# Kernel tuning notes

Hardware: AMD Instinct MI355X
Metric: run time of the kernel (lower is better)

Reference implementation:

```python
import jax, jax.numpy as jnp
import numpy as np

B, T, D_IN, H, BR, D_OUT = 256, 500, 700, 200, 2, 35
V_TH = 1.0


def setup_inputs() -> dict:
    key = jax.random.key(0)
    ks = jax.random.split(key, 7)
    x = jax.random.normal(ks[0], (B, T, D_IN), dtype=jnp.float32)
    W_in = jax.random.normal(ks[1], (H * BR, D_IN), dtype=jnp.float32) * (1.0 / np.sqrt(D_IN))
    b_in = jax.random.normal(ks[2], (H * BR,), dtype=jnp.float32) * 0.01
    # tau_n ~ U(0, 4) per branch per neuron (as in SimpleDH_LIF init)
    tau_n = jax.random.uniform(ks[3], (H, BR), dtype=jnp.float32, minval=0.0, maxval=4.0)
    tau_m = jnp.full((H,), 2.0, dtype=jnp.float32)  # torch init: tensor(2.0) per neuron
    W_out = jax.random.normal(ks[5], (D_OUT, H), dtype=jnp.float32) * (1.0 / np.sqrt(H))
    b_out = jax.random.normal(ks[6], (D_OUT,), dtype=jnp.float32) * 0.01
    return {"x": x, "W_in": W_in, "b_in": b_in, "tau_n": tau_n,
            "tau_m": tau_m, "W_out": W_out, "b_out": b_out}


def reference(x, W_in, b_in, tau_n, tau_m, W_out, b_out):
    b, t, _ = x.shape
    # Batched input projection for all timesteps at once: (B,T,H*BR) -> (T,B,H,BR)
    branch_in = jnp.einsum('bti,oi->bto', x, W_in) + b_in
    branch_in = branch_in.reshape(b, t, H, BR).transpose(1, 0, 2, 3)

    beta = jax.nn.sigmoid(tau_n)          # (H, BR) dendritic branch decay
    alpha = jax.nn.sigmoid(tau_m)         # (H,)   soma membrane decay

    def step(carry, inp_t):
        v, i_d, counts = carry            # v:(B,H) i_d:(B,H,BR) counts:(B,H)
        i_d = beta * i_d + (1.0 - beta) * inp_t
        i_total = i_d.sum(axis=-1)        # (B,H)
        v = alpha * v + (1.0 - alpha) * i_total
        spike = (v >= V_TH).astype(v.dtype)
        v = v - spike * V_TH
        return (v, i_d, counts + spike), None

    v0 = jnp.zeros((b, H), dtype=x.dtype)
    i0 = jnp.zeros((b, H, BR), dtype=x.dtype)
    c0 = jnp.zeros((b, H), dtype=x.dtype)
    (v, i_d, spike_counts), _ = jax.lax.scan(step, (v0, i0, c0), branch_in)

    return spike_counts @ W_out.T + b_out  # (B, D_OUT)
```

## Files before the change

kernel.cpp:

```cpp
#include <hip/hip_runtime.h>

#define B_   256
#define T_   500
#define DIN  700
#define H_   200
#define NO   400
#define DOUT 35
#define NKC  22

typedef _Float16 half_t;
typedef __attribute__((ext_vector_type(8))) _Float16 half8;
typedef __attribute__((ext_vector_type(4))) float floatx4;

#define SX 16.0f
#define SW 4096.0f
#define INV_S (1.0f / 65536.0f)

__device__ __forceinline__ float sigmoidf_(float x) {
    return 1.0f / (1.0f + expf(-x));
}

__global__ __launch_bounds__(256) void cvt_wfrag(
    const float* __restrict__ W, half_t* __restrict__ Whf, half_t* __restrict__ Wlf)
{
    int t = blockIdx.x * 256 + threadIdx.x;
    if (t >= NKC * 25 * 64) return;
    int lane = t & 63;
    int rest = t >> 6;
    int nfg  = rest % 25;
    int kc   = rest / 25;
    int la = lane & 15, lb = lane >> 4;
    int row = nfg * 16 + la;
    int col = kc * 32 + lb * 8;
    half8 hh, ll;
    #pragma unroll
    for (int j = 0; j < 8; ++j) {
        float v = (col + j < DIN) ? W[(size_t)row * DIN + col + j] : 0.0f;
        float s = v * SW;
        half_t h = (half_t)s;
        hh[j] = h;
        ll[j] = (half_t)(s - (float)h);
    }
    *reinterpret_cast<half8*>(&Whf[(size_t)t * 8]) = hh;
    *reinterpret_cast<half8*>(&Wlf[(size_t)t * 8]) = ll;
}

__global__ __launch_bounds__(256, 1) void dh_gemm_ovl(
    const float* __restrict__ x,
    const half_t* __restrict__ Whf, const half_t* __restrict__ Wlf,
    const float* __restrict__ bin, float* __restrict__ Y)
{
    int p = blockIdx.x;
    int xcd = p & 7, slot = p >> 3;
    int L = (xcd < 4 ? xcd * 313 : 4 * 313 + (xcd - 4) * 312) + slot;

    const int w    = threadIdx.x >> 6;
    const int lane = threadIdx.x & 63;
    const int la   = lane & 15;
    const int lb   = lane >> 4;

    const int wave = L * 4 + w;
    const int mt = wave / 5, nt = wave - mt * 5;
    const int m0 = mt * 64;
    const int o0 = nt * 80;

    floatx4 acc[4][5];
    #pragma unroll
    for (int mf = 0; mf < 4; ++mf)
        #pragma unroll
        for (int nf = 0; nf < 5; ++nf) {
            floatx4 z = {0.f, 0.f, 0.f, 0.f};
            acc[mf][nf] = z;
        }

    size_t arow[4];
    #pragma unroll
    for (int mf = 0; mf < 4; ++mf)
        arow[mf] = (size_t)(m0 + mf * 16 + la) * DIN;
    const size_t bbase = ((size_t)(nt * 5) * 64 + lane) * 8;

    float4 aE[4][2], aO[4][2];
    half8 bEh[5], bEl[5], bOh[5], bOl[5];
    half8 fEh[4], fEl[4], fOh[4], fOl[4];

    auto LOADA = [&](float4 (&ra)[4][2], int kc) {
        if (kc > NKC - 1) kc = NKC - 1;
        const int col = kc * 32 + lb * 8;
        const int c2ofs = (col + 8 <= DIN) ? 4 : (692 - col);
        #pragma unroll
        for (int mf = 0; mf < 4; ++mf) {
            const float* ptr = &x[arow[mf] + col];
            ra[mf][0] = *reinterpret_cast<const float4*>(ptr);
            ra[mf][1] = *reinterpret_cast<const float4*>(ptr + c2ofs);
        }
    };
    auto LOADB = [&](half8 (&bh)[5], half8 (&bl)[5], int kc) {
        if (kc > NKC - 1) kc = NKC - 1;
        const size_t kofs = (size_t)kc * 25 * 64 * 8;
        #pragma unroll
        for (int nf = 0; nf < 5; ++nf) {
            size_t idx = bbase + kofs + (size_t)nf * 64 * 8;
            bh[nf] = *reinterpret_cast<const half8*>(&Whf[idx]);
            bl[nf] = *reinterpret_cast<const half8*>(&Wlf[idx]);
        }
    };
    auto CONV = [&](half8 (&fh)[4], half8 (&fl)[4], const float4 (&ra)[4][2]) {
        #pragma unroll
        for (int mf = 0; mf < 4; ++mf) {
            float vv[8];
            *reinterpret_cast<float4*>(&vv[0]) = ra[mf][0];
            *reinterpret_cast<float4*>(&vv[4]) = ra[mf][1];
            half8 hh, ll;
            #pragma unroll
            for (int j = 0; j < 8; ++j) {
                float s = vv[j] * SX;
                half_t h = (half_t)s;
                hh[j] = h;
                ll[j] = (half_t)(s - (float)h);
            }
            fh[mf] = hh;
            fl[mf] = ll;
        }
    };
    auto MFMAS = [&](const half8 (&fh)[4], const half8 (&fl)[4],
                     const half8 (&bh)[5], const half8 (&bl)[5]) {
        #pragma unroll
        for (int mf = 0; mf < 4; ++mf)
            #pragma unroll
            for (int nf = 0; nf < 5; ++nf)
                acc[mf][nf] = __builtin_amdgcn_mfma_f32_16x16x32_f16(fh[mf], bh[nf], acc[mf][nf], 0, 0, 0);
        #pragma unroll
        for (int mf = 0; mf < 4; ++mf)
            #pragma unroll
            for (int nf = 0; nf < 5; ++nf)
                acc[mf][nf] = __builtin_amdgcn_mfma_f32_16x16x32_f16(fh[mf], bl[nf], acc[mf][nf], 0, 0, 0);
        #pragma unroll
        for (int mf = 0; mf < 4; ++mf)
            #pragma unroll
            for (int nf = 0; nf < 5; ++nf)
                acc[mf][nf] = __builtin_amdgcn_mfma_f32_16x16x32_f16(fl[mf], bh[nf], acc[mf][nf], 0, 0, 0);
    };

#define SBAR() __builtin_amdgcn_sched_barrier(0)

    LOADA(aE, 0); SBAR();
    LOADB(bEh, bEl, 0); SBAR();
    LOADA(aO, 1); SBAR();
    LOADB(bOh, bOl, 1); SBAR();
    CONV(fEh, fEl, aE);
    SBAR();
    LOADA(aE, 2);
    SBAR();

    #pragma unroll 1
    for (int I = 0; I < 10; ++I) {
        const int kc = 2 * I;
        MFMAS(fEh, fEl, bEh, bEl);
        CONV(fOh, fOl, aO);
        SBAR();
        LOADB(bEh, bEl, kc + 2); SBAR();
        LOADA(aO, kc + 3); SBAR();
        MFMAS(fOh, fOl, bOh, bOl);
        CONV(fEh, fEl, aE);
        SBAR();
        LOADB(bOh, bOl, kc + 3); SBAR();
        LOADA(aE, kc + 4); SBAR();
    }
    MFMAS(fEh, fEl, bEh, bEl);
    CONV(fOh, fOl, aO);
    SBAR();
    MFMAS(fOh, fOl, bOh, bOl);

    float bo[5];
    #pragma unroll
    for (int nf = 0; nf < 5; ++nf) bo[nf] = bin[o0 + nf * 16 + la];

    #pragma unroll
    for (int mf = 0; mf < 4; ++mf) {
        int mbase = m0 + mf * 16 + lb * 4;
        #pragma unroll
        for (int rg = 0; rg < 4; ++rg) {
            int mm = mbase + rg;
            int bb = mm / T_;
            int tt = mm - bb * T_;
            float* yrow = &Y[((size_t)tt * B_ + bb) * NO + o0 + la];
            #pragma unroll
            for (int nf = 0; nf < 5; ++nf)
                yrow[nf * 16] = acc[mf][nf][rg] * INV_S + bo[nf];
        }
    }
#undef SBAR
}

#define BM 256
#define BN 64
#define BK 16
__global__ __launch_bounds__(256) void dh_gemm_in(
    const float* __restrict__ x, const float* __restrict__ Wt,
    const float* __restrict__ bin, float* __restrict__ Y)
{
    __shared__ float As[BK][BM + 4];
    __shared__ float Bs[BK][BN + 4];
    const int tid = threadIdx.x;
    const int tx = tid & 7;
    const int ty = tid >> 3;
    const int m0 = blockIdx.y * BM;
    const int o0 = blockIdx.x * BN;

    float acc[8][8];
    #pragma unroll
    for (int r = 0; r < 8; ++r)
        #pragma unroll
        for (int c = 0; c < 8; ++c) acc[r][c] = 0.0f;

    const int srow = tid >> 2;
    const int skq  = (tid & 3) << 2;

    for (int k0 = 0; k0 < DIN; k0 += BK) {
        float4 areg[4];
        #pragma unroll
        for (int i = 0; i < 4; ++i) {
            int idx = tid + i * 256;
            int row = idx >> 2;
            int kq  = (idx & 3) << 2;
            int kg  = k0 + kq;
            if (kg < DIN)
                areg[i] = *reinterpret_cast<const float4*>(&x[(size_t)(m0 + row) * DIN + kg]);
            else
                areg[i] = make_float4(0.f, 0.f, 0.f, 0.f);
        }
        float4 breg;
        {
            int kg = k0 + skq;
            int o  = o0 + srow;
            if (kg < DIN && o < NO)
                breg = *reinterpret_cast<const float4*>(&Wt[(size_t)o * DIN + kg]);
            else
                breg = make_float4(0.f, 0.f, 0.f, 0.f);
        }
        __syncthreads();
        #pragma unroll
        for (int i = 0; i < 4; ++i) {
            int idx = tid + i * 256;
            int row = idx >> 2;
            int kq  = (idx & 3) << 2;
            As[kq + 0][row] = areg[i].x;
            As[kq + 1][row] = areg[i].y;
            As[kq + 2][row] = areg[i].z;
            As[kq + 3][row] = areg[i].w;
        }
        Bs[skq + 0][srow] = breg.x;
        Bs[skq + 1][srow] = breg.y;
        Bs[skq + 2][srow] = breg.z;
        Bs[skq + 3][srow] = breg.w;
        __syncthreads();

        #pragma unroll
        for (int k = 0; k < BK; ++k) {
            float a[8], bb[8];
            *reinterpret_cast<float4*>(&a[0])  = *reinterpret_cast<const float4*>(&As[k][ty * 8]);
            *reinterpret_cast<float4*>(&a[4])  = *reinterpret_cast<const float4*>(&As[k][ty * 8 + 4]);
            *reinterpret_cast<float4*>(&bb[0]) = *reinterpret_cast<const float4*>(&Bs[k][tx * 8]);
            *reinterpret_cast<float4*>(&bb[4]) = *reinterpret_cast<const float4*>(&Bs[k][tx * 8 + 4]);
            #pragma unroll
            for (int r = 0; r < 8; ++r)
                #pragma unroll
                for (int c = 0; c < 8; ++c)
                    acc[r][c] = fmaf(a[r], bb[c], acc[r][c]);
        }
    }

    float bo[8];
    #pragma unroll
    for (int c = 0; c < 8; ++c) {
        int o = o0 + tx * 8 + c;
        bo[c] = (o < NO) ? bin[o] : 0.0f;
    }
    const int ob = o0 + tx * 8;
    if (ob < NO) {
        #pragma unroll
        for (int r = 0; r < 8; ++r) {
            int m = m0 + ty * 8 + r;
            int b = m / T_;
            int t = m - b * T_;
            float* yrow = &Y[((size_t)t * B_ + b) * NO];
            float4 v0 = make_float4(acc[r][0] + bo[0], acc[r][1] + bo[1],
                                    acc[r][2] + bo[2], acc[r][3] + bo[3]);
            float4 v1 = make_float4(acc[r][4] + bo[4], acc[r][5] + bo[5],
                                    acc[r][6] + bo[6], acc[r][7] + bo[7]);
            *reinterpret_cast<float4*>(&yrow[ob])     = v0;
            *reinterpret_cast<float4*>(&yrow[ob + 4]) = v1;
        }
    }
}

__global__ __launch_bounds__(64) void dh_scan(
    const float* __restrict__ Y, const float* __restrict__ tau_n,
    const float* __restrict__ tau_m, float* __restrict__ counts)
{
    int g = blockIdx.x * 64 + threadIdx.x;
    int b = g / H_;
    int h = g - b * H_;
    (void)b;
    float beta0 = sigmoidf_(tau_n[h * 2 + 0]);
    float beta1 = sigmoidf_(tau_n[h * 2 + 1]);
    float alpha = sigmoidf_(tau_m[h]);
    float omb0 = 1.0f - beta0, omb1 = 1.0f - beta1, oma = 1.0f - alpha;
    const float2* Yp = reinterpret_cast<const float2*>(Y);

    float v = 0.f, i0 = 0.f, i1 = 0.f, cnt = 0.f;
    #pragma unroll 1
    for (int t0 = 0; t0 < T_; t0 += 10) {
        float2 yb[10];
        #pragma unroll
        for (int j = 0; j < 10; ++j)
            yb[j] = Yp[(size_t)(t0 + j) * (B_ * H_) + g];
        #pragma unroll
        for (int j = 0; j < 10; ++j) {
            i0 = beta0 * i0 + omb0 * yb[j].x;
            i1 = beta1 * i1 + omb1 * yb[j].y;
            float it = i0 + i1;
            v = alpha * v + oma * it;
            if (v >= 1.0f) { v -= 1.0f; cnt += 1.0f; }
        }
    }
    counts[g] = cnt;
}

__global__ __launch_bounds__(64) void dh_out(
    const float* __restrict__ counts, const float* __restrict__ W_out,
    const float* __restrict__ b_out, float* __restrict__ out)
{
    int b = blockIdx.x;
    int o = threadIdx.x;
    if (o >= DOUT) return;
    float acc = b_out[o];
    const float* c = &counts[(size_t)b * H_];
    const float* w = &W_out[(size_t)o * H_];
    #pragma unroll 4
    for (int h = 0; h < H_; ++h)
        acc = fmaf(c[h], w[h], acc);
    out[(size_t)b * DOUT + o] = acc;
}

extern "C" void kernel_launch(void* const* d_in, const int* in_sizes, int n_in,
                              void* d_out, int out_size, void* d_ws, size_t ws_size,
                              hipStream_t stream) {
    const float* x     = (const float*)d_in[0];
    const float* W_in  = (const float*)d_in[1];
    const float* b_in  = (const float*)d_in[2];
    const float* tau_n = (const float*)d_in[3];
    const float* tau_m = (const float*)d_in[4];
    const float* W_out = (const float*)d_in[5];
    const float* b_out = (const float*)d_in[6];
    float* out = (float*)d_out;

    float* Y      = (float*)d_ws;
    float* counts = Y + (size_t)T_ * B_ * NO;

    const size_t nfrag_halves = (size_t)NKC * 25 * 64 * 8;
    size_t need = ((size_t)T_ * B_ * NO + (size_t)B_ * H_) * 4
                + 2 * nfrag_halves * 2;

    if (ws_size >= need) {
        half_t* Whf = (half_t*)(counts + (size_t)B_ * H_);
        half_t* Wlf = Whf + nfrag_halves;

        cvt_wfrag<<<(NKC * 25 * 64 + 255) / 256, 256, 0, stream>>>(W_in, Whf, Wlf);
        dh_gemm_ovl<<<2500, 256, 0, stream>>>(x, Whf, Wlf, b_in, Y);
    } else {
        dim3 g1(7, 500);
        dh_gemm_in<<<g1, 256, 0, stream>>>(x, W_in, b_in, Y);
    }

    dh_scan<<<(B_ * H_) / 64, 64, 0, stream>>>(Y, tau_n, tau_m, counts);
    dh_out<<<B_, 64, 0, stream>>>(counts, W_out, b_out, out);
}
```

Baseline: 396.8 us.

## Fuse fp16 split conversion into MFMA loop to fit two workgroups per CU

Raises launch bounds to two workgroups per CU and cuts register pressure to make that fit. It drops the separate converted-fragment buffers and converts each A row fragment just before its MFMAs, and it uses 32-bit offsets instead of size_t. The software pipeline is restructured to prefetch raw loads only, with the loop now running 11 iterations. The aim is more waves per CU to hide memory latency, at the cost of less explicit overlap between conversion and MFMA within a wave, and possible register spills.

```diff
diff --git a/kernel.cpp b/kernel.cpp
--- a/kernel.cpp
+++ b/kernel.cpp
@@ -45,7 +45,7 @@
     *reinterpret_cast<half8*>(&Wlf[(size_t)t * 8]) = ll;
 }
 
-__global__ __launch_bounds__(256, 1) void dh_gemm_ovl(
+__global__ __launch_bounds__(256, 2) void dh_gemm_2wb(
     const float* __restrict__ x,
     const half_t* __restrict__ Whf, const half_t* __restrict__ Wlf,
     const float* __restrict__ bin, float* __restrict__ Y)
@@ -73,15 +73,14 @@
             acc[mf][nf] = z;
         }
 
-    size_t arow[4];
+    unsigned arow[4];
     #pragma unroll
     for (int mf = 0; mf < 4; ++mf)
-        arow[mf] = (size_t)(m0 + mf * 16 + la) * DIN;
-    const size_t bbase = ((size_t)(nt * 5) * 64 + lane) * 8;
+        arow[mf] = (unsigned)(m0 + mf * 16 + la) * DIN;
+    const unsigned bbase = (unsigned)((nt * 5) * 64 + lane) * 8;
 
     float4 aE[4][2], aO[4][2];
     half8 bEh[5], bEl[5], bOh[5], bOl[5];
-    half8 fEh[4], fEl[4], fOh[4], fOl[4];
 
     auto LOADA = [&](float4 (&ra)[4][2], int kc) {
         if (kc > NKC - 1) kc = NKC - 1;
@@ -89,56 +88,47 @@
         const int c2ofs = (col + 8 <= DIN) ? 4 : (692 - col);
         #pragma unroll
         for (int mf = 0; mf < 4; ++mf) {
-            const float* ptr = &x[arow[mf] + col];
+            const float* ptr = x + arow[mf] + col;
             ra[mf][0] = *reinterpret_cast<const float4*>(ptr);
             ra[mf][1] = *reinterpret_cast<const float4*>(ptr + c2ofs);
         }
     };
     auto LOADB = [&](half8 (&bh)[5], half8 (&bl)[5], int kc) {
         if (kc > NKC - 1) kc = NKC - 1;
-        const size_t kofs = (size_t)kc * 25 * 64 * 8;
+        const unsigned kofs = (unsigned)kc * 12800;
         #pragma unroll
         for (int nf = 0; nf < 5; ++nf) {
-            size_t idx = bbase + kofs + (size_t)nf * 64 * 8;
-            bh[nf] = *reinterpret_cast<const half8*>(&Whf[idx]);
-            bl[nf] = *reinterpret_cast<const half8*>(&Wlf[idx]);
+            unsigned idx = bbase + kofs + (unsigned)nf * 512;
+            bh[nf] = *reinterpret_cast<const half8*>(Whf + idx);
+            bl[nf] = *reinterpret_cast<const half8*>(Wlf + idx);
         }
     };
-    auto CONV = [&](half8 (&fh)[4], half8 (&fl)[4], const float4 (&ra)[4][2]) {
+    auto CMFMA = [&](const float4 (&ra)[4][2],
+                     const half8 (&bh)[5], const half8 (&bl)[5]) {
         #pragma unroll
         for (int mf = 0; mf < 4; ++mf) {
+            __builtin_amdgcn_sched_barrier(0);
             float vv[8];
             *reinterpret_cast<float4*>(&vv[0]) = ra[mf][0];
             *reinterpret_cast<float4*>(&vv[4]) = ra[mf][1];
-            half8 hh, ll;
+            half8 ah, al;
             #pragma unroll
             for (int j = 0; j < 8; ++j) {
                 float s = vv[j] * SX;
                 half_t h = (half_t)s;
-                hh[j] = h;
-                ll[j] = (half_t)(s - (float)h);
+                ah[j] = h;
+                al[j] = (half_t)(s - (float)h);
             }
-            fh[mf] = hh;
-            fl[mf] = ll;
-        }
-    };
-    auto MFMAS = [&](const half8 (&fh)[4], const half8 (&fl)[4],
-                     const half8 (&bh)[5], const half8 (&bl)[5]) {
-        #pragma unroll
-        for (int mf = 0; mf < 4; ++mf)
             #pragma unroll
             for (int nf = 0; nf < 5; ++nf)
-                acc[mf][nf] = __builtin_amdgcn_mfma_f32_16x16x32_f16(fh[mf], bh[nf], acc[mf][nf], 0, 0, 0);
-        #pragma unroll
-        for (int mf = 0; mf < 4; ++mf)
+                acc[mf][nf] = __builtin_amdgcn_mfma_f32_16x16x32_f16(ah, bh[nf], acc[mf][nf], 0, 0, 0);
             #pragma unroll
             for (int nf = 0; nf < 5; ++nf)
-                acc[mf][nf] = __builtin_amdgcn_mfma_f32_16x16x32_f16(fh[mf], bl[nf], acc[mf][nf], 0, 0, 0);
-        #pragma unroll
-        for (int mf = 0; mf < 4; ++mf)
+                acc[mf][nf] = __builtin_amdgcn_mfma_f32_16x16x32_f16(ah, bl[nf], acc[mf][nf], 0, 0, 0);
             #pragma unroll
             for (int nf = 0; nf < 5; ++nf)
-                acc[mf][nf] = __builtin_amdgcn_mfma_f32_16x16x32_f16(fl[mf], bh[nf], acc[mf][nf], 0, 0, 0);
+                acc[mf][nf] = __builtin_amdgcn_mfma_f32_16x16x32_f16(al, bh[nf], acc[mf][nf], 0, 0, 0);
+        }
     };
 
 #define SBAR() __builtin_amdgcn_sched_barrier(0)
@@ -147,29 +137,23 @@
     LOADB(bEh, bEl, 0); SBAR();
     LOADA(aO, 1); SBAR();
     LOADB(bOh, bOl, 1); SBAR();
-    CONV(fEh, fEl, aE);
-    SBAR();
-    LOADA(aE, 2);
-    SBAR();
 
     #pragma unroll 1
-    for (int I = 0; I < 10; ++I) {
+    for (int I = 0; I < 11; ++I) {
         const int kc = 2 * I;
-        MFMAS(fEh, fEl, bEh, bEl);
-        CONV(fOh, fOl, aO);
-        SBAR();
-        LOADB(bEh, bEl, kc + 2); SBAR();
-        LOADA(aO, kc + 3); SBAR();
-        MFMAS(fOh, fOl, bOh, bOl);
-        CONV(fEh, fEl, aE);
-        SBAR();
-        LOADB(bOh, bOl, kc + 3); SBAR();
-        LOADA(aE, kc + 4); SBAR();
-    }
-    MFMAS(fEh, fEl, bEh, bEl);
-    CONV(fOh, fOl, aO);
-    SBAR();
-    MFMAS(fOh, fOl, bOh, bOl);
+        SBAR();
+        CMFMA(aE, bEh, bEl);
+        SBAR();
+        LOADA(aE, kc + 2);
+        SBAR();
+        LOADB(bEh, bEl, kc + 2);
+        SBAR();
+        CMFMA(aO, bOh, bOl);
+        SBAR();
+        LOADA(aO, kc + 3);
+        SBAR();
+        LOADB(bOh, bOl, kc + 3);
+    }
 
     float bo[5];
     #pragma unroll
@@ -367,7 +351,7 @@
         half_t* Wlf = Whf + nfrag_halves;
 
         cvt_wfrag<<<(NKC * 25 * 64 + 255) / 256, 256, 0, stream>>>(W_in, Whf, Wlf);
-        dh_gemm_ovl<<<2500, 256, 0, stream>>>(x, Whf, Wlf, b_in, Y);
+        dh_gemm_2wb<<<2500, 256, 0, stream>>>(x, Whf, Wlf, b_in, Y);
     } else {
         dim3 g1(7, 500);
         dh_gemm_in<<<g1, 256, 0, stream>>>(x, W_in, b_in, Y);
```

After: 393.9 us. Within noise of the previous version (-0.7%).
